# Kernel optimization log

Hardware: AMD Instinct MI355X
Metric: run time of the kernel (lower is better)

## Reference

```python
import jax, jax.numpy as jnp
import numpy as np

B, H, E, V, K = 1024, 128, 16, 100000, 512

def setup_inputs() -> dict:
    key = jax.random.key(0)
    k1, k2, k3, k4, k5 = jax.random.split(key, 5)
    return {
        "h": jax.random.normal(k1, (B, H), dtype=jnp.float32),
        "valid_indices": jax.random.randint(k2, (B, K), 0, V, dtype=jnp.int32),
        "word_embeddings": jax.random.normal(k3, (V, E), dtype=jnp.float32),
        "W": jax.random.normal(k4, (E, H), dtype=jnp.float32) * (1.0 / np.sqrt(H)),
        "b": jax.random.normal(k5, (E,), dtype=jnp.float32) * 0.01,
    }

def reference(h, valid_indices, word_embeddings, W, b):
    # linear projection: [B,H] @ [H,E] + [E] -> [B,E]
    query = h @ W.T + b
    # scores: [B,E] @ [E,V] -> [B,V]
    scores = jnp.einsum('be,ve->bv', query, word_embeddings)
    # boolean valid mask via one batched scatter (replaces per-row python loop)
    rows = jnp.arange(B, dtype=jnp.int32)[:, None]              # [B,1]
    valid = jnp.zeros((B, V), dtype=bool).at[rows, valid_indices].set(True)
    # invalid positions get -inf added (equivalent to scores + where(mask,-inf,0))
    return jnp.where(valid, scores, -jnp.inf)
```

## Files before the change

### kernel.cpp

```cpp
#include <hip/hip_runtime.h>
#include <math.h>

#define PB 1024
#define PH 128
#define PE 16
#define PV 100000
#define PK 512

#define MASKED_PAIR  (0xFBFFFBFFu)

static constexpr int MASK_WORDS = (PV + 31) / 32;
static constexpr int CHUNK      = (MASK_WORDS + 255) / 256;

union Pack8 {
    uint4 u4;
    unsigned short s[8];
};

__global__ __launch_bounds__(256) void PolicyHead_68685116998378_kernel(
    const float* __restrict__ h,
    const int*   __restrict__ valid_idx,
    const float* __restrict__ emb,
    const float* __restrict__ W,
    const float* __restrict__ bias,
    unsigned short* __restrict__ out)
{
    __shared__ unsigned int   mask[MASK_WORDS];
    __shared__ unsigned short prefix[MASK_WORDS];
    __shared__ unsigned short scorev[PK];
    __shared__ float partials[256];
    __shared__ float query[PE];
    __shared__ unsigned int wavesum[4];

    const int b = blockIdx.x;
    const int t = threadIdx.x;

    for (int i = t; i < MASK_WORDS; i += 256) mask[i] = 0u;
    {
        const int e = t & 15;
        const int j = t >> 4;
        const float* hrow = h + b * PH + j * 8;
        const float* wrow = W + e * PH + j * 8;
        float s = 0.f;
        #pragma unroll
        for (int i = 0; i < 8; ++i) s += hrow[i] * wrow[i];
        partials[t] = s;
    }
    __syncthreads();

    for (int k = t; k < PK; k += 256) {
        unsigned int idx = (unsigned int)valid_idx[b * PK + k];
        if (idx < PV) atomicOr(&mask[idx >> 5], 1u << (idx & 31));
    }
    if (t < PE) {
        float s = bias[t];
        #pragma unroll
        for (int j = 0; j < 16; ++j) s += partials[j * 16 + t];
        query[t] = s;
    }
    __syncthreads();

    const int cs = t * CHUNK;
    const int ce = (cs + CHUNK < MASK_WORDS) ? cs + CHUNK : MASK_WORDS;
    unsigned int csum = 0;
    for (int j = cs; j < ce; ++j) csum += __popc(mask[j]);
    unsigned int x = csum;
    #pragma unroll
    for (int d = 1; d < 64; d <<= 1) {
        unsigned int y = __shfl_up(x, d, 64);
        if ((t & 63) >= d) x += y;
    }
    if ((t & 63) == 63) wavesum[t >> 6] = x;
    __syncthreads();
    unsigned int waveoff = 0;
    for (int w = 0; w < (t >> 6); ++w) waveoff += wavesum[w];
    unsigned int run = waveoff + x - csum;
    for (int j = cs; j < ce; ++j) {
        prefix[j] = (unsigned short)run;
        run += __popc(mask[j]);
    }
    __syncthreads();

    float q[PE];
    #pragma unroll
    for (int i = 0; i < PE; ++i) q[i] = query[i];

    for (int k = t; k < PK; k += 256) {
        unsigned int idx = (unsigned int)valid_idx[b * PK + k];
        if (idx < PV) {
            const unsigned int w = mask[idx >> 5];
            const unsigned int rank =
                prefix[idx >> 5] + __popc(w & ((1u << (idx & 31)) - 1u));
            const float* erow = emb + (size_t)idx * PE;
            float s = 0.f;
            #pragma unroll
            for (int i = 0; i < PE; ++i) s += q[i] * erow[i];
            s = (fabsf(s) < 1e30f) ? s : 0.0f;
            unsigned int fb = __builtin_bit_cast(unsigned int, s);
            fb += 0x7FFFu + ((fb >> 16) & 1u);
            scorev[rank] = (unsigned short)(fb >> 16);
        }
    }
    __syncthreads();

    unsigned short* orow = out + (size_t)b * PV;
    const int n8 = PV / 8;
    for (int c = t; c < n8; c += 256) {
        const int v = c * 8;
        const unsigned int word = mask[v >> 5];
        const unsigned int bits = (word >> (v & 31)) & 0xFFu;
        Pack8 r;
        r.u4 = make_uint4(MASKED_PAIR, MASKED_PAIR, MASKED_PAIR, MASKED_PAIR);
        if (bits) {
            const unsigned int base =
                prefix[v >> 5] + __popc(word & ((1u << (v & 31)) - 1u));
            #pragma unroll
            for (int u = 0; u < 8; ++u) {
                if (bits & (1u << u)) {
                    r.s[u] = scorev[base + __popc(bits & ((1u << u) - 1u))];
                }
            }
        }
        *(uint4*)(orow + v) = r.u4;
    }
}

extern "C" void kernel_launch(void* const* d_in, const int* in_sizes, int n_in,
                              void* d_out, int out_size, void* d_ws, size_t ws_size,
                              hipStream_t stream) {
    const float* h    = (const float*)d_in[0];
    const int*   vi   = (const int*)  d_in[1];
    const float* emb  = (const float*)d_in[2];
    const float* W    = (const float*)d_in[3];
    const float* bias = (const float*)d_in[4];
    unsigned short* out = (unsigned short*)d_out;

    PolicyHead_68685116998378_kernel<<<dim3(PB), dim3(256), 0, stream>>>(
        h, vi, emb, W, bias, out);
}
```

Before: 383.3 us.

## Split each row's vocabulary into four blocks and use nontemporal output stores

Each batch row is now handled by four blocks, one per quarter of the vocabulary. Each block builds only its local mask, prefix sums and scores and writes its slice of the output. This gives four times as many blocks and a smaller shared-memory footprint, for better occupancy and more parallelism on the store-bound output write. The cost is redundant query projection and index loads in each of the four blocks. It also preloads the two indices per thread, switches the scatter loop to bit iteration, and uses nontemporal vector stores for the output.

```diff
diff --git a/kernel.cpp b/kernel.cpp
--- a/kernel.cpp
+++ b/kernel.cpp
@@ -9,11 +9,15 @@
 
 #define MASKED_PAIR  (0xFBFFFBFFu)
 
-static constexpr int MASK_WORDS = (PV + 31) / 32;
-static constexpr int CHUNK      = (MASK_WORDS + 255) / 256;
+typedef unsigned int u32x4 __attribute__((ext_vector_type(4)));
+
+static constexpr int GSPLIT = 4;
+static constexpr int VSUB   = PV / GSPLIT;
+static constexpr int MWL    = (VSUB + 31) / 32;
+static constexpr int CHUNK  = (MWL + 255) / 256;
 
 union Pack8 {
-    uint4 u4;
+    u32x4 u4;
     unsigned short s[8];
 };
 
@@ -25,17 +29,20 @@
     const float* __restrict__ bias,
     unsigned short* __restrict__ out)
 {
-    __shared__ unsigned int   mask[MASK_WORDS];
-    __shared__ unsigned short prefix[MASK_WORDS];
+    __shared__ unsigned int   mask[MWL];
+    __shared__ unsigned short prefix[MWL];
     __shared__ unsigned short scorev[PK];
     __shared__ float partials[256];
     __shared__ float query[PE];
     __shared__ unsigned int wavesum[4];
 
-    const int b = blockIdx.x;
+    const int bid = blockIdx.x;
+    const int b   = bid >> 2;
+    const int g   = bid & (GSPLIT - 1);
+    const unsigned int vbase = (unsigned int)(g * VSUB);
     const int t = threadIdx.x;
 
-    for (int i = t; i < MASK_WORDS; i += 256) mask[i] = 0u;
+    for (int i = t; i < MWL; i += 256) mask[i] = 0u;
     {
         const int e = t & 15;
         const int j = t >> 4;
@@ -46,11 +53,15 @@
         for (int i = 0; i < 8; ++i) s += hrow[i] * wrow[i];
         partials[t] = s;
     }
+    const unsigned int idx0 = (unsigned int)valid_idx[b * PK + t];
+    const unsigned int idx1 = (unsigned int)valid_idx[b * PK + t + 256];
     __syncthreads();
 
-    for (int k = t; k < PK; k += 256) {
-        unsigned int idx = (unsigned int)valid_idx[b * PK + k];
-        if (idx < PV) atomicOr(&mask[idx >> 5], 1u << (idx & 31));
+    {
+        const unsigned int l0 = idx0 - vbase;
+        if (l0 < (unsigned int)VSUB) atomicOr(&mask[l0 >> 5], 1u << (l0 & 31));
+        const unsigned int l1 = idx1 - vbase;
+        if (l1 < (unsigned int)VSUB) atomicOr(&mask[l1 >> 5], 1u << (l1 & 31));
     }
     if (t < PE) {
         float s = bias[t];
@@ -61,7 +72,7 @@
     __syncthreads();
 
     const int cs = t * CHUNK;
-    const int ce = (cs + CHUNK < MASK_WORDS) ? cs + CHUNK : MASK_WORDS;
+    const int ce = (cs + CHUNK < MWL) ? cs + CHUNK : MWL;
     unsigned int csum = 0;
     for (int j = cs; j < ce; ++j) csum += __popc(mask[j]);
     unsigned int x = csum;
@@ -85,12 +96,14 @@
     #pragma unroll
     for (int i = 0; i < PE; ++i) q[i] = query[i];
 
-    for (int k = t; k < PK; k += 256) {
-        unsigned int idx = (unsigned int)valid_idx[b * PK + k];
-        if (idx < PV) {
-            const unsigned int w = mask[idx >> 5];
+    #pragma unroll
+    for (int kk = 0; kk < 2; ++kk) {
+        const unsigned int idx = kk ? idx1 : idx0;
+        const unsigned int l = idx - vbase;
+        if (l < (unsigned int)VSUB) {
+            const unsigned int w = mask[l >> 5];
             const unsigned int rank =
-                prefix[idx >> 5] + __popc(w & ((1u << (idx & 31)) - 1u));
+                prefix[l >> 5] + __popc(w & ((1u << (l & 31)) - 1u));
             const float* erow = emb + (size_t)idx * PE;
             float s = 0.f;
             #pragma unroll
@@ -103,25 +116,25 @@
     }
     __syncthreads();
 
-    unsigned short* orow = out + (size_t)b * PV;
-    const int n8 = PV / 8;
+    unsigned short* orow = out + (size_t)b * PV + vbase;
+    const int n8 = VSUB / 8;
     for (int c = t; c < n8; c += 256) {
         const int v = c * 8;
         const unsigned int word = mask[v >> 5];
         const unsigned int bits = (word >> (v & 31)) & 0xFFu;
         Pack8 r;
-        r.u4 = make_uint4(MASKED_PAIR, MASKED_PAIR, MASKED_PAIR, MASKED_PAIR);
+        r.u4 = (u32x4){MASKED_PAIR, MASKED_PAIR, MASKED_PAIR, MASKED_PAIR};
         if (bits) {
             const unsigned int base =
                 prefix[v >> 5] + __popc(word & ((1u << (v & 31)) - 1u));
-            #pragma unroll
-            for (int u = 0; u < 8; ++u) {
-                if (bits & (1u << u)) {
-                    r.s[u] = scorev[base + __popc(bits & ((1u << u) - 1u))];
-                }
+            unsigned int bb = bits;
+            while (bb) {
+                const int u = __builtin_ctz(bb);
+                bb &= bb - 1u;
+                r.s[u] = scorev[base + __popc(bits & ((1u << u) - 1u))];
             }
         }
-        *(uint4*)(orow + v) = r.u4;
+        __builtin_nontemporal_store(r.u4, (u32x4*)(orow + v));
     }
 }
 
@@ -135,6 +148,6 @@
     const float* bias = (const float*)d_in[4];
     unsigned short* out = (unsigned short*)d_out;
 
-    PolicyHead_68685116998378_kernel<<<dim3(PB), dim3(256), 0, stream>>>(
+    PolicyHead_68685116998378_kernel<<<dim3(PB * GSPLIT), dim3(256), 0, stream>>>(
         h, vi, emb, W, bias, out);
 }
```

New measurement: 395.2 us. 1.03x slower.
